# Optimization experiments

Hardware: AMD Instinct MI355X
Metric: run time of the kernel (lower is better)

The kernel has to match this reference:

```python
import jax, jax.numpy as jnp
import numpy as np

# Dimensions
B = 2          # batch
WIN = 8
S = WIN * WIN  # 64 tokens in the window
C = 64         # embed_dim (per-head channel dim)
NH = 8         # num_heads
H, W = 32, 32  # per-token spatial field
M1, M2 = 16, 16  # retained Fourier modes


def _spectral_conv(x, w):
    """FNO-style spectral conv over the last two dims.
    x: [B, S, Cin, H, W] real; w: [Cin, Cout, M1, M2, 2] (real/imag parts).
    rfft2 -> truncate to (M1, M2) modes -> complex channel mixing -> irfft2.
    """
    wc = w[..., 0] + 1j * w[..., 1]                      # [Cin, Cout, M1, M2]
    xf = jnp.fft.rfft2(x)                                # [B, S, Cin, H, W//2+1]
    of = jnp.einsum('bsixy,ioxy->bsoxy', xf[..., :M1, :M2], wc)
    out_f = jnp.zeros(xf.shape[:2] + (wc.shape[1], H, W // 2 + 1), dtype=of.dtype)
    out_f = out_f.at[..., :M1, :M2].set(of)
    return jnp.fft.irfft2(out_f, s=(H, W))               # [B, S, Cout, H, W]


def _log_cpb(w1, b1, w2, b2):
    """Swin-v2 style log-spaced continuous position bias.
    MLP(2 -> C -> NH) on log-spaced relative coords of the WIN x WIN window.
    Returns [NH, S, S].
    """
    g = jnp.arange(WIN)
    coords = jnp.stack(jnp.meshgrid(g, g, indexing='ij'), 0).reshape(2, -1)   # [2, S]
    rel = (coords[:, :, None] - coords[:, None, :]).astype(jnp.float32)       # [2, S, S]
    rel = jnp.transpose(rel, (1, 2, 0)) * (8.0 / (WIN - 1))                   # [S, S, 2]
    rel = jnp.sign(rel) * jnp.log2(jnp.abs(rel) + 1.0) / np.float32(np.log2(8.0))
    h = jax.nn.relu(rel @ w1 + b1)                                            # [S, S, C]
    bias = h @ w2 + b2                                                        # [S, S, NH]
    return 16.0 * jax.nn.sigmoid(jnp.transpose(bias, (2, 0, 1)))              # [NH, S, S]


def setup_inputs() -> dict:
    key = jax.random.key(0)
    k = jax.random.split(key, 8)
    def rn(kk, shape, s):
        return jax.random.normal(kk, shape, jnp.float32) * np.float32(s)
    return {
        'seq': jax.random.normal(k[0], (B, S, C, H, W), jnp.float32),
        'wq': rn(k[1], (C, C * NH, M1, M2, 2), 1.0 / C),
        'wk': rn(k[2], (C, C * NH, M1, M2, 2), 1.0 / C),
        'wv': rn(k[3], (C, C * NH, M1, M2, 2), 1.0 / C),
        'wo': rn(k[4], (C * NH, C, M1, M2, 2), 1.0 / (C * NH)),
        'cpb_w1': rn(k[5], (2, C), 0.1),
        'cpb_b1': jnp.zeros((C,), jnp.float32),
        'cpb_w2': rn(k[6], (C, NH), 0.1),
        'cpb_b2': jnp.zeros((NH,), jnp.float32),
    }


def reference(seq, wq, wk, wv, wo, cpb_w1, cpb_b1, cpb_w2, cpb_b2):
    # Spectral QKV projections: C -> NH*C channels
    q = _spectral_conv(seq, wq)   # [B, S, NH*C, H, W]
    kk = _spectral_conv(seq, wk)
    v = _spectral_conv(seq, wv)

    def unfl(f):  # [B, S, NH*C, H, W] -> [B, NH, S, C, H, W]
        return jnp.transpose(f.reshape(B, S, NH, C, H, W), (0, 2, 1, 3, 4, 5))

    q, kk, v = unfl(q), unfl(kk), unfl(v)

    bias = _log_cpb(cpb_w1, cpb_b1, cpb_w2, cpb_b2)      # [NH, S, S]
    scale = np.float32(1.0 / np.sqrt(C * H * W))
    scores = jnp.einsum('bhsdxy,bhtdxy->bhst', q, kk) * scale + bias
    attn = jax.nn.softmax(scores, axis=-1)               # [B, NH, S, S]
    o = jnp.einsum('bhst,bhtdxy->bhsdxy', attn, v)       # [B, NH, S, C, H, W]

    o = jnp.transpose(o, (0, 2, 1, 3, 4, 5)).reshape(B, S, NH * C, H, W)
    return _spectral_conv(o, wo)                         # [B, S, C, H, W]
```

## Files before the change

kernel.cpp:

```cpp
#include <hip/hip_runtime.h>
#include <math.h>


#define PI_F 3.14159265358979323846f

typedef _Float16 f16;
typedef f16 f16x8 __attribute__((ext_vector_type(8)));
typedef f16 f16x4 __attribute__((ext_vector_type(4)));
typedef float f32x4 __attribute__((ext_vector_type(4)));

#define MFMA(a, b, c) __builtin_amdgcn_mfma_f32_16x16x32_f16(a, b, c, 0, 0, 0)

__device__ __forceinline__ int swz128(int row, int slot) {
  return (row << 7) + (((slot) ^ (row & 7)) << 4);
}
__device__ __forceinline__ int swzel(int row, int col) {
  return (row << 7) + ((((col) >> 3) ^ (row & 7)) << 4) + (((col) & 7) << 1);
}

__device__ void dft_body(char* sm, int f, int tid, const float* __restrict__ seq,
                         f16* __restrict__ Xr, f16* __restrict__ Xi) {
  float(*fld)[33] = (float(*)[33])sm;
  float2(*tb)[17] = (float2(*)[17])(sm + 4224);
  float2* tw = (float2*)(sm + 8576);
  if (tid < 32) {
    float a = (2.0f * PI_F / 32.0f) * (float)tid;
    tw[tid] = make_float2(cosf(a), sinf(a));
  }
  const float4* s4 = (const float4*)(seq + (size_t)f * 1024);
  float4 v = s4[tid];
  int x0 = tid >> 3, y0 = (tid & 7) * 4;
  fld[x0][y0 + 0] = v.x; fld[x0][y0 + 1] = v.y;
  fld[x0][y0 + 2] = v.z; fld[x0][y0 + 3] = v.w;
  __syncthreads();
  for (int o = tid; o < 512; o += 256) {
    int x = o >> 4, q = o & 15;
    float re = 0.f, im = 0.f;
#pragma unroll
    for (int y = 0; y < 32; ++y) {
      float val = fld[x][y];
      float2 w = tw[(q * y) & 31];
      re = fmaf(val, w.x, re);
      im = fmaf(val, -w.y, im);
    }
    tb[x][q] = make_float2(re, im);
  }
  __syncthreads();
  int p = tid >> 4, q = tid & 15;
  float re = 0.f, im = 0.f;
#pragma unroll
  for (int x = 0; x < 32; ++x) {
    float2 t = tb[x][q];
    float2 w = tw[(p * x) & 31];
    re += w.x * t.x + w.y * t.y;
    im += w.x * t.y - w.y * t.x;
  }
  int b = f >> 12;
  int si = f & 4095;
  size_t o = (size_t)(b * 256 + tid) * 4096 + si;
  Xr[o] = (f16)re;
  Xi[o] = (f16)im;
}

__device__ void repack_body(char* sm, int gid, int tid,
                            const float2* __restrict__ wq,
                            const float2* __restrict__ wk,
                            const float2* __restrict__ wv,
                            const float2* __restrict__ wo,
                            f16* __restrict__ Pqr, f16* __restrict__ Pqi,
                            f16* __restrict__ Pkr, f16* __restrict__ Pki,
                            f16* __restrict__ Pvr, f16* __restrict__ Pvi,
                            f16* __restrict__ Por, f16* __restrict__ Poi) {
  f16(*tR)[72] = (f16(*)[72])sm;
  f16(*tI)[72] = (f16(*)[72])(sm + 9216);
  int tsel = gid >> 11, r = gid & 2047;
  const float2* in;
  f16 *oR, *oI;
  int m0 = (r & 3) * 64, a0, bb, A, B;
  bool scaled = (tsel == 0) || (tsel == 2);
  if (tsel == 3) {
    in = wo; oR = Por; oI = Poi;
    a0 = ((r >> 2) & 7) * 64; bb = r >> 5; A = 512; B = 64;
  } else {
    a0 = 0; bb = r >> 2; A = 64; B = 512;
    in = (tsel == 0) ? wq : (tsel == 1) ? wk : wv;
    oR = (tsel == 0) ? Pqr : (tsel == 1) ? Pkr : Pvr;
    oI = (tsel == 0) ? Pqi : (tsel == 1) ? Pki : Pvi;
  }
  const float4* in4 = (const float4*)in;
  for (int k = tid; k < 2048; k += 256) {
    int ai = k >> 5, mj = k & 31;
    float4 v = in4[((size_t)(a0 + ai) * B + bb) * 128 + (m0 >> 1) + mj];
    int sw = (mj & 7) << 3;
    tR[2 * mj + 0][ai ^ sw] = (f16)v.x;
    tI[2 * mj + 0][ai ^ sw] = (f16)v.y;
    tR[2 * mj + 1][ai ^ sw] = (f16)v.z;
    tI[2 * mj + 1][ai ^ sw] = (f16)v.w;
  }
  __syncthreads();
  for (int k = tid; k < 1024; k += 256) {
    int pl = k >> 9, s = k & 511;
    int mi = s >> 3, a8 = (s & 7) * 8;
    int sw = ((mi >> 1) & 7) << 3;
    f16x8 v = pl ? *(const f16x8*)&tI[mi][a8 ^ sw]
                 : *(const f16x8*)&tR[mi][a8 ^ sw];
    int mode = m0 + mi;
    if (scaled) {
      f16 scl = (mode == 0) ? (f16)1.0f
                            : (((mode & 15) == 0) ? (f16)0.5f : (f16)2.0f);
      v = v * scl;
      if (pl && mode == 0) v = (f16x8)(f16)0.0f;
    }
    f16* dst = pl ? oI : oR;
    *(f16x8*)&dst[(size_t)mode * 32768 + (size_t)bb * A + a0 + a8] = v;
  }
}

__global__ __launch_bounds__(256) void k_mega(
    const float* __restrict__ seq, f16* __restrict__ Xr, f16* __restrict__ Xi,
    const float2* __restrict__ wq, const float2* __restrict__ wk,
    const float2* __restrict__ wv, const float2* __restrict__ wo,
    f16* __restrict__ Pqr, f16* __restrict__ Pqi, f16* __restrict__ Pkr,
    f16* __restrict__ Pki, f16* __restrict__ Pvr, f16* __restrict__ Pvi,
    f16* __restrict__ Por, f16* __restrict__ Poi) {
  __shared__ __align__(16) char sm[18432];
  int orig = blockIdx.x, tid = threadIdx.x;
  if (orig < 8192) {
    int gid = (orig & 7) * 1024 + (orig >> 3);
    repack_body(sm, gid, tid, wq, wk, wv, wo, Pqr, Pqi, Pkr, Pki, Pvr, Pvi,
                Por, Poi);
  } else {
    dft_body(sm, orig - 8192, tid, seq, Xr, Xi);
  }
}

__global__ __launch_bounds__(256, 2) void k_scores_m(
    const f16* __restrict__ Xr, const f16* __restrict__ Xi,
    const f16* __restrict__ Qwr, const f16* __restrict__ Qwi,
    const f16* __restrict__ Kwr, const f16* __restrict__ Kwi,
    float* __restrict__ scores) {
  __shared__ __align__(16) unsigned char smem[65536];
  const int P_WQR = 0, P_WQI = 8192, P_WKR = 16384, P_WKI = 24576;
  const int P_QR = 32768, P_QI = 40960, P_KR = 49152, P_KI = 57344;
  int tid = threadIdx.x;
  int w = tid >> 6, lane = tid & 63, r = lane & 15, g = lane >> 4;
  int wr = w >> 1, wc = w & 1;
  int chunk = blockIdx.x, h = blockIdx.y;
  f32x4 S[2][2][2] = {};
  for (int mm = 0; mm < 4; ++mm) {
    int m = chunk * 4 + mm;
    const float4* gqr = (const float4*)Qwr + (size_t)m * 4096 + h * 512;
    const float4* gqi = (const float4*)Qwi + (size_t)m * 4096 + h * 512;
    const float4* gkr = (const float4*)Kwr + (size_t)m * 4096 + h * 512;
    const float4* gki = (const float4*)Kwi + (size_t)m * 4096 + h * 512;
#pragma unroll
    for (int it = 0; it < 2; ++it) {
      int s = tid + it * 256;
      int lo = swz128(s >> 3, s & 7);
      *(float4*)(smem + P_WQR + lo) = gqr[s];
      *(float4*)(smem + P_WQI + lo) = gqi[s];
      *(float4*)(smem + P_WKR + lo) = gkr[s];
      *(float4*)(smem + P_WKI + lo) = gki[s];
    }
    __syncthreads();
#pragma unroll
    for (int b = 0; b < 2; ++b) {
      const f16x8* xr8 = (const f16x8*)Xr + (size_t)(b * 256 + m) * 512;
      const f16x8* xi8 = (const f16x8*)Xi + (size_t)(b * 256 + m) * 512;
      f16x8 axr[2][2], axi[2][2];
#pragma unroll
      for (int rt = 0; rt < 2; ++rt)
#pragma unroll
        for (int kt = 0; kt < 2; ++kt) {
          int idx = (32 * wr + rt * 16 + r) * 8 + kt * 4 + g;
          axr[rt][kt] = xr8[idx];
          axi[rt][kt] = xi8[idx];
        }
      {
        f32x4 cr[2][2] = {}, ci[2][2] = {};
#pragma unroll
        for (int ct = 0; ct < 2; ++ct)
#pragma unroll
          for (int kt = 0; kt < 2; ++kt) {
            int lo = swz128(32 * wc + ct * 16 + r, kt * 4 + g);
            f16x8 bwr = *(const f16x8*)(smem + P_WQR + lo);
            f16x8 bwi = *(const f16x8*)(smem + P_WQI + lo);
            f16x8 bwiN = -bwi;
#pragma unroll
            for (int rt = 0; rt < 2; ++rt) {
              cr[rt][ct] = MFMA(axr[rt][kt], bwr, cr[rt][ct]);
              cr[rt][ct] = MFMA(axi[rt][kt], bwiN, cr[rt][ct]);
              ci[rt][ct] = MFMA(axr[rt][kt], bwi, ci[rt][ct]);
              ci[rt][ct] = MFMA(axi[rt][kt], bwr, ci[rt][ct]);
            }
          }
#pragma unroll
        for (int rt = 0; rt < 2; ++rt)
#pragma unroll
          for (int ct = 0; ct < 2; ++ct)
#pragma unroll
            for (int j = 0; j < 4; ++j) {
              int row = 32 * wr + rt * 16 + g * 4 + j;
              int col = 32 * wc + ct * 16 + r;
              *(f16*)(smem + P_QR + swzel(row, col)) = (f16)cr[rt][ct][j];
              *(f16*)(smem + P_QI + swzel(row, col)) = (f16)ci[rt][ct][j];
            }
      }
      {
        f32x4 cr[2][2] = {}, ci[2][2] = {};
#pragma unroll
        for (int ct = 0; ct < 2; ++ct)
#pragma unroll
          for (int kt = 0; kt < 2; ++kt) {
            int lo = swz128(32 * wc + ct * 16 + r, kt * 4 + g);
            f16x8 bwr = *(const f16x8*)(smem + P_WKR + lo);
            f16x8 bwi = *(const f16x8*)(smem + P_WKI + lo);
            f16x8 bwiN = -bwi;
#pragma unroll
            for (int rt = 0; rt < 2; ++rt) {
              cr[rt][ct] = MFMA(axr[rt][kt], bwr, cr[rt][ct]);
              cr[rt][ct] = MFMA(axi[rt][kt], bwiN, cr[rt][ct]);
              ci[rt][ct] = MFMA(axr[rt][kt], bwi, ci[rt][ct]);
              ci[rt][ct] = MFMA(axi[rt][kt], bwr, ci[rt][ct]);
            }
          }
#pragma unroll
        for (int rt = 0; rt < 2; ++rt)
#pragma unroll
          for (int ct = 0; ct < 2; ++ct)
#pragma unroll
            for (int j = 0; j < 4; ++j) {
              int row = 32 * wr + rt * 16 + g * 4 + j;
              int col = 32 * wc + ct * 16 + r;
              *(f16*)(smem + P_KR + swzel(row, col)) = (f16)cr[rt][ct][j];
              *(f16*)(smem + P_KI + swzel(row, col)) = (f16)ci[rt][ct][j];
            }
      }
      __syncthreads();
      {
        f16x8 aqr[2][2], aqi[2][2];
#pragma unroll
        for (int rt = 0; rt < 2; ++rt)
#pragma unroll
          for (int kt = 0; kt < 2; ++kt) {
            int lo = swz128(32 * wr + rt * 16 + r, kt * 4 + g);
            aqr[rt][kt] = *(const f16x8*)(smem + P_QR + lo);
            aqi[rt][kt] = *(const f16x8*)(smem + P_QI + lo);
          }
#pragma unroll
        for (int ct = 0; ct < 2; ++ct)
#pragma unroll
          for (int kt = 0; kt < 2; ++kt) {
            int lo = swz128(32 * wc + ct * 16 + r, kt * 4 + g);
            f16x8 bkr = *(const f16x8*)(smem + P_KR + lo);
            f16x8 bki = *(const f16x8*)(smem + P_KI + lo);
#pragma unroll
            for (int rt = 0; rt < 2; ++rt) {
              S[b][rt][ct] = MFMA(aqr[rt][kt], bkr, S[b][rt][ct]);
              S[b][rt][ct] = MFMA(aqi[rt][kt], bki, S[b][rt][ct]);
            }
          }
      }
      __syncthreads();
    }
  }
  const float fac = 1.0f / 262144.0f;
#pragma unroll
  for (int b = 0; b < 2; ++b) {
    float* dst = scores + ((size_t)(b * 8 + h)) * 4096;
#pragma unroll
    for (int rt = 0; rt < 2; ++rt)
#pragma unroll
      for (int ct = 0; ct < 2; ++ct)
#pragma unroll
        for (int j = 0; j < 4; ++j) {
          int s_ = 32 * wr + rt * 16 + g * 4 + j;
          int t_ = 32 * wc + ct * 16 + r;
          atomicAdd(&dst[s_ * 64 + t_], S[b][rt][ct][j] * fac);
        }
  }
}

__global__ __launch_bounds__(64) void k_softmax(const float* __restrict__ scores,
                                                const float* __restrict__ w1,
                                                const float* __restrict__ b1,
                                                const float* __restrict__ w2,
                                                const float* __restrict__ b2,
                                                f16* __restrict__ at) {
  int id = blockIdx.x;
  int s = id & 63;
  int h = (id >> 6) & 7;
  int t = threadIdx.x;
  float d0 = (float)((s >> 3) - (t >> 3)) * (8.0f / 7.0f);
  float d1 = (float)((s & 7) - (t & 7)) * (8.0f / 7.0f);
  float a0 = log2f(fabsf(d0) + 1.0f) * (1.0f / 3.0f);
  float a1 = log2f(fabsf(d1) + 1.0f) * (1.0f / 3.0f);
  float r0 = (d0 < 0.f) ? -a0 : a0;
  float r1 = (d1 < 0.f) ? -a1 : a1;
  float acc = b2[h];
  for (int c = 0; c < 64; ++c) {
    float hv = fmaf(r0, w1[c], fmaf(r1, w1[64 + c], b1[c]));
    hv = fmaxf(hv, 0.0f);
    acc = fmaf(hv, w2[c * 8 + h], acc);
  }
  float bias = 16.0f / (1.0f + expf(-acc));
  size_t base = (size_t)id * 64;
  float v = scores[base + t] + bias;
  float mx = v;
  for (int o = 32; o; o >>= 1) mx = fmaxf(mx, __shfl_xor(mx, o));
  float e = expf(v - mx);
  float sm = e;
  for (int o = 32; o; o >>= 1) sm += __shfl_xor(sm, o);
  at[base + t] = (f16)(e / sm);
}

__global__ __launch_bounds__(256, 2) void k_vpath_m(
    const f16* __restrict__ Xr, const f16* __restrict__ Xi,
    const f16* __restrict__ Vwr, const f16* __restrict__ Vwi,
    const f16* __restrict__ Owr, const f16* __restrict__ Owi,
    const f16* __restrict__ At, float2* __restrict__ Ff) {
  __shared__ __align__(16) unsigned char smem[73728];
  const int P_WVR = 0, P_WVI = 8192, P_WOR = 16384, P_WOI = 24576;
  const int P_VTR = 32768, P_VTI = 40960, P_YR = 49152, P_YI = 57344;
  const int P_AT = 65536;
  int tid = threadIdx.x;
  int w = tid >> 6, lane = tid & 63, r = lane & 15, g = lane >> 4;
  int wr = w >> 1, wc = w & 1;
  int m = blockIdx.x, b = blockIdx.y;
  const f16x8* xr8 = (const f16x8*)Xr + (size_t)(b * 256 + m) * 512;
  const f16x8* xi8 = (const f16x8*)Xi + (size_t)(b * 256 + m) * 512;
  f16x8 axr[2][2], axi[2][2], axiN[2][2];
#pragma unroll
  for (int rt = 0; rt < 2; ++rt)
#pragma unroll
    for (int kt = 0; kt < 2; ++kt) {
      int idx = (32 * wr + rt * 16 + r) * 8 + kt * 4 + g;
      axr[rt][kt] = xr8[idx];
      axi[rt][kt] = xi8[idx];
      axiN[rt][kt] = -axi[rt][kt];
    }
  f32x4 fr[2][2] = {}, fi_[2][2] = {};
  for (int h = 0; h < 8; ++h) {
    __syncthreads();
    const float4* gvr = (const float4*)Vwr + (size_t)m * 4096 + h * 512;
    const float4* gvi = (const float4*)Vwi + (size_t)m * 4096 + h * 512;
    const float4* gor = (const float4*)Owr + (size_t)m * 4096 + h * 8;
    const float4* goi = (const float4*)Owi + (size_t)m * 4096 + h * 8;
    const float4* gat = (const float4*)At + (size_t)(b * 8 + h) * 512;
#pragma unroll
    for (int it = 0; it < 2; ++it) {
      int s = tid + it * 256;
      int row = s >> 3, sl = s & 7;
      int lo = swz128(row, sl);
      *(float4*)(smem + P_WVR + lo) = gvr[s];
      *(float4*)(smem + P_WVI + lo) = gvi[s];
      *(float4*)(smem + P_WOR + lo) = gor[row * 64 + sl];
      *(float4*)(smem + P_WOI + lo) = goi[row * 64 + sl];
      *(float4*)(smem + P_AT + lo) = gat[s];
    }
    __syncthreads();
    {
      f32x4 vr[2][2] = {}, vi[2][2] = {};
#pragma unroll
      for (int ct = 0; ct < 2; ++ct)
#pragma unroll
        for (int kt = 0; kt < 2; ++kt) {
          int lo = swz128(32 * wc + ct * 16 + r, kt * 4 + g);
          f16x8 bwr = *(const f16x8*)(smem + P_WVR + lo);
          f16x8 bwi = *(const f16x8*)(smem + P_WVI + lo);
#pragma unroll
          for (int rt = 0; rt < 2; ++rt) {
            vr[rt][ct] = MFMA(axr[rt][kt], bwr, vr[rt][ct]);
            vr[rt][ct] = MFMA(axiN[rt][kt], bwi, vr[rt][ct]);
            vi[rt][ct] = MFMA(axr[rt][kt], bwi, vi[rt][ct]);
            vi[rt][ct] = MFMA(axi[rt][kt], bwr, vi[rt][ct]);
          }
        }
#pragma unroll
      for (int rt = 0; rt < 2; ++rt)
#pragma unroll
        for (int ct = 0; ct < 2; ++ct) {
          int drow = 32 * wc + ct * 16 + r;
          int t0 = 32 * wr + rt * 16 + g * 4;
          f16x4 pr, pi;
#pragma unroll
          for (int j = 0; j < 4; ++j) {
            pr[j] = (f16)vr[rt][ct][j];
            pi[j] = (f16)vi[rt][ct][j];
          }
          int lo = swzel(drow, t0);
          *(f16x4*)(smem + P_VTR + lo) = pr;
          *(f16x4*)(smem + P_VTI + lo) = pi;
        }
    }
    __syncthreads();
    {
      f16x8 aat[2][2];
#pragma unroll
      for (int rt = 0; rt < 2; ++rt)
#pragma unroll
        for (int kt = 0; kt < 2; ++kt)
          aat[rt][kt] = *(const f16x8*)(
              smem + P_AT + swz128(32 * wr + rt * 16 + r, kt * 4 + g));
      f32x4 yr[2][2] = {}, yi[2][2] = {};
#pragma unroll
      for (int ct = 0; ct < 2; ++ct)
#pragma unroll
        for (int kt = 0; kt < 2; ++kt) {
          int lo = swz128(32 * wc + ct * 16 + r, kt * 4 + g);
          f16x8 bvr = *(const f16x8*)(smem + P_VTR + lo);
          f16x8 bvi = *(const f16x8*)(smem + P_VTI + lo);
#pragma unroll
          for (int rt = 0; rt < 2; ++rt) {
            yr[rt][ct] = MFMA(aat[rt][kt], bvr, yr[rt][ct]);
            yi[rt][ct] = MFMA(aat[rt][kt], bvi, yi[rt][ct]);
          }
        }
#pragma unroll
      for (int rt = 0; rt < 2; ++rt)
#pragma unroll
        for (int ct = 0; ct < 2; ++ct)
#pragma unroll
          for (int j = 0; j < 4; ++j) {
            int row = 32 * wr + rt * 16 + g * 4 + j;
            int col = 32 * wc + ct * 16 + r;
            *(f16*)(smem + P_YR + swzel(row, col)) = (f16)yr[rt][ct][j];
            *(f16*)(smem + P_YI + swzel(row, col)) = (f16)yi[rt][ct][j];
          }
    }
    __syncthreads();
    {
      f16x8 ayr[2][2], ayi[2][2], ayiN[2][2];
#pragma unroll
      for (int rt = 0; rt < 2; ++rt)
#pragma unroll
        for (int kt = 0; kt < 2; ++kt) {
          int lo = swz128(32 * wr + rt * 16 + r, kt * 4 + g);
          ayr[rt][kt] = *(const f16x8*)(smem + P_YR + lo);
          ayi[rt][kt] = *(const f16x8*)(smem + P_YI + lo);
          ayiN[rt][kt] = -ayi[rt][kt];
        }
#pragma unroll
      for (int ct = 0; ct < 2; ++ct)
#pragma unroll
        for (int kt = 0; kt < 2; ++kt) {
          int lo = swz128(32 * wc + ct * 16 + r, kt * 4 + g);
          f16x8 bor = *(const f16x8*)(smem + P_WOR + lo);
          f16x8 boi = *(const f16x8*)(smem + P_WOI + lo);
#pragma unroll
          for (int rt = 0; rt < 2; ++rt) {
            fr[rt][ct] = MFMA(ayr[rt][kt], bor, fr[rt][ct]);
            fr[rt][ct] = MFMA(ayiN[rt][kt], boi, fr[rt][ct]);
            fi_[rt][ct] = MFMA(ayr[rt][kt], boi, fi_[rt][ct]);
            fi_[rt][ct] = MFMA(ayi[rt][kt], bor, fi_[rt][ct]);
          }
        }
    }
  }
#pragma unroll
  for (int rt = 0; rt < 2; ++rt)
#pragma unroll
    for (int ct = 0; ct < 2; ++ct)
#pragma unroll
      for (int j = 0; j < 4; ++j) {
        int s_ = 32 * wr + rt * 16 + g * 4 + j;
        int c_ = 32 * wc + ct * 16 + r;
        Ff[(((size_t)(b * 64 + s_)) * 64 + c_) * 256 + m] =
            make_float2(fr[rt][ct][j], fi_[rt][ct][j]);
      }
}

__global__ __launch_bounds__(256) void k_idft(const float2* __restrict__ Ff,
                                              float* __restrict__ out) {
  __shared__ float2 Fm[256];
  __shared__ float2 g[32][17];
  __shared__ float2 tw[32];
  int f = blockIdx.x;
  int tid = threadIdx.x;
  if (tid < 32) {
    float a = (2.0f * PI_F / 32.0f) * (float)tid;
    tw[tid] = make_float2(cosf(a), sinf(a));
  }
  Fm[tid] = Ff[(size_t)f * 256 + tid];
  __syncthreads();
  for (int o = tid; o < 512; o += 256) {
    int x = o >> 4, q = o & 15;
    float gr = 0.f, gi = 0.f;
#pragma unroll
    for (int p = 0; p < 16; ++p) {
      float2 a = Fm[p * 16 + q];
      float2 w = tw[(p * x) & 31];
      gr += a.x * w.x - a.y * w.y;
      gi += a.x * w.y + a.y * w.x;
    }
    g[x][q] = make_float2(gr, gi);
  }
  __syncthreads();
  int x = tid >> 3, j0 = (tid & 7) * 4;
  float4 r;
  float* rr = &r.x;
#pragma unroll
  for (int jj = 0; jj < 4; ++jj) {
    int j = j0 + jj;
    float acc = 0.f;
#pragma unroll
    for (int q = 0; q < 16; ++q) {
      float2 gv = g[x][q];
      float2 w = tw[(q * j) & 31];
      acc += gv.x * w.x - gv.y * w.y;
    }
    rr[jj] = acc * (1.0f / 1024.0f);
  }
  *(float4*)(out + (size_t)f * 1024 + x * 32 + j0) = r;
}

extern "C" void kernel_launch(void* const* d_in, const int* in_sizes, int n_in,
                              void* d_out, int out_size, void* d_ws,
                              size_t ws_size, hipStream_t stream) {
  const float* seq = (const float*)d_in[0];
  const float2* wq = (const float2*)d_in[1];
  const float2* wk = (const float2*)d_in[2];
  const float2* wv = (const float2*)d_in[3];
  const float2* wo = (const float2*)d_in[4];
  const float* w1 = (const float*)d_in[5];
  const float* b1 = (const float*)d_in[6];
  const float* w2 = (const float*)d_in[7];
  const float* b2 = (const float*)d_in[8];
  float* out = (float*)d_out;

  char* ws = (char*)d_ws;
  f16* Xr = (f16*)(ws + 0);
  f16* Xi = (f16*)(ws + 4194304);
  float* scores = (float*)(ws + 8388608);
  f16* At = (f16*)(ws + 8650752);
  float2* Ff = (float2*)(ws + 8781824);
  f16* Pqr = (f16*)(ws + 25559040);
  f16* Pqi = (f16*)(ws + 42336256);
  f16* Pkr = (f16*)(ws + 59113472);
  f16* Pki = (f16*)(ws + 75890688);
  f16* Pvr = (f16*)(ws + 92667904);
  f16* Pvi = (f16*)(ws + 109445120);
  f16* Por = (f16*)(ws + 126222336);
  f16* Poi = (f16*)(ws + 142999552);

  hipMemsetAsync(scores, 0, 262144, stream);
  k_mega<<<16384, 256, 0, stream>>>(seq, Xr, Xi, wq, wk, wv, wo, Pqr, Pqi,
                                    Pkr, Pki, Pvr, Pvi, Por, Poi);
  k_scores_m<<<dim3(64, 8), 256, 0, stream>>>(Xr, Xi, Pqr, Pqi, Pkr, Pki,
                                              scores);
  k_softmax<<<1024, 64, 0, stream>>>(scores, w1, b1, w2, b2, At);
  k_vpath_m<<<dim3(256, 2), 256, 0, stream>>>(Xr, Xi, Pvr, Pvi, Por, Poi, At,
                                              Ff);
  k_idft<<<8192, 256, 0, stream>>>(Ff, out);
}
```

Measured before the change: 264.5 us.

## Transpose Ff to mode-major layout and remap vpath block order

k_vpath_m now writes its spectral outputs mode-major, so each block stores a contiguous 64x64 tile instead of stride-256 scattered float2 writes. k_idft then gathers its 256 modes with a stride of 8192 elements. The vpath grid is flattened and remapped so that blocks with adjacent ids cover groups of 8 modes for both batches. The mega kernel also drops its block-id interleave for the repack part. This trades coalesced reads in idft for coalesced writes in vpath, and changes the block scheduling order for L2 locality.

```diff
diff --git a/kernel.cpp b/kernel.cpp
--- a/kernel.cpp
+++ b/kernel.cpp
@@ -124,13 +124,12 @@
     f16* __restrict__ Pki, f16* __restrict__ Pvr, f16* __restrict__ Pvi,
     f16* __restrict__ Por, f16* __restrict__ Poi) {
   __shared__ __align__(16) char sm[18432];
-  int orig = blockIdx.x, tid = threadIdx.x;
-  if (orig < 8192) {
-    int gid = (orig & 7) * 1024 + (orig >> 3);
-    repack_body(sm, gid, tid, wq, wk, wv, wo, Pqr, Pqi, Pkr, Pki, Pvr, Pvi,
+  int bx = blockIdx.x, tid = threadIdx.x;
+  if (bx < 8192) {
+    repack_body(sm, bx, tid, wq, wk, wv, wo, Pqr, Pqi, Pkr, Pki, Pvr, Pvi,
                 Por, Poi);
   } else {
-    dft_body(sm, orig - 8192, tid, seq, Xr, Xi);
+    dft_body(sm, bx - 8192, tid, seq, Xr, Xi);
   }
 }
 
@@ -318,7 +317,7 @@
     const f16* __restrict__ Xr, const f16* __restrict__ Xi,
     const f16* __restrict__ Vwr, const f16* __restrict__ Vwi,
     const f16* __restrict__ Owr, const f16* __restrict__ Owi,
-    const f16* __restrict__ At, float2* __restrict__ Ff) {
+    const f16* __restrict__ At, float2* __restrict__ Ff2) {
   __shared__ __align__(16) unsigned char smem[73728];
   const int P_WVR = 0, P_WVI = 8192, P_WOR = 16384, P_WOI = 24576;
   const int P_VTR = 32768, P_VTI = 40960, P_YR = 49152, P_YI = 57344;
@@ -326,7 +325,9 @@
   int tid = threadIdx.x;
   int w = tid >> 6, lane = tid & 63, r = lane & 15, g = lane >> 4;
   int wr = w >> 1, wc = w & 1;
-  int m = blockIdx.x, b = blockIdx.y;
+  int id = blockIdx.x;
+  int m = ((id >> 4) << 3) + (id & 7);
+  int b = (id >> 3) & 1;
   const f16x8* xr8 = (const f16x8*)Xr + (size_t)(b * 256 + m) * 512;
   const f16x8* xi8 = (const f16x8*)Xi + (size_t)(b * 256 + m) * 512;
   f16x8 axr[2][2], axi[2][2], axiN[2][2];
@@ -457,6 +458,7 @@
         }
     }
   }
+  float2* dst = Ff2 + (size_t)m * 8192 + (size_t)b * 4096;
 #pragma unroll
   for (int rt = 0; rt < 2; ++rt)
 #pragma unroll
@@ -465,12 +467,11 @@
       for (int j = 0; j < 4; ++j) {
         int s_ = 32 * wr + rt * 16 + g * 4 + j;
         int c_ = 32 * wc + ct * 16 + r;
-        Ff[(((size_t)(b * 64 + s_)) * 64 + c_) * 256 + m] =
-            make_float2(fr[rt][ct][j], fi_[rt][ct][j]);
+        dst[s_ * 64 + c_] = make_float2(fr[rt][ct][j], fi_[rt][ct][j]);
       }
 }
 
-__global__ __launch_bounds__(256) void k_idft(const float2* __restrict__ Ff,
+__global__ __launch_bounds__(256) void k_idft(const float2* __restrict__ Ff2,
                                               float* __restrict__ out) {
   __shared__ float2 Fm[256];
   __shared__ float2 g[32][17];
@@ -481,7 +482,7 @@
     float a = (2.0f * PI_F / 32.0f) * (float)tid;
     tw[tid] = make_float2(cosf(a), sinf(a));
   }
-  Fm[tid] = Ff[(size_t)f * 256 + tid];
+  Fm[tid] = Ff2[(size_t)tid * 8192 + f];
   __syncthreads();
   for (int o = tid; o < 512; o += 256) {
     int x = o >> 4, q = o & 15;
@@ -533,7 +534,7 @@
   f16* Xi = (f16*)(ws + 4194304);
   float* scores = (float*)(ws + 8388608);
   f16* At = (f16*)(ws + 8650752);
-  float2* Ff = (float2*)(ws + 8781824);
+  float2* Ff2 = (float2*)(ws + 8781824);
   f16* Pqr = (f16*)(ws + 25559040);
   f16* Pqi = (f16*)(ws + 42336256);
   f16* Pkr = (f16*)(ws + 59113472);
@@ -549,7 +550,6 @@
   k_scores_m<<<dim3(64, 8), 256, 0, stream>>>(Xr, Xi, Pqr, Pqi, Pkr, Pki,
                                               scores);
   k_softmax<<<1024, 64, 0, stream>>>(scores, w1, b1, w2, b2, At);
-  k_vpath_m<<<dim3(256, 2), 256, 0, stream>>>(Xr, Xi, Pvr, Pvi, Por, Poi, At,
-                                              Ff);
-  k_idft<<<8192, 256, 0, stream>>>(Ff, out);
-}
+  k_vpath_m<<<512, 256, 0, stream>>>(Xr, Xi, Pvr, Pvi, Por, Poi, At, Ff2);
+  k_idft<<<8192, 256, 0, stream>>>(Ff2, out);
+}
```

Result: faster. 233.7 us, median of 2 (-11.6%).
